# Kernel optimization log

Hardware: AMD Instinct MI355X
Metric: run time of the kernel (lower is better)

Reference implementation:

```python
import jax, jax.numpy as jnp
import numpy as np

N = 50000      # nodes
E = 800000     # directed edges (before self loops)
B = 64         # graphs in batch
F_IN = 128     # input_dim
POS = 16       # pos_dim
H = 4          # heads
C = 64         # hidden_dim (per head)
HC = H * C     # 256
OUT = 128      # output_dim
ENH = F_IN + POS
EPS = 1e-5
NEG_SLOPE = 0.2


def setup_inputs() -> dict:
    key = jax.random.key(0)
    ks = jax.random.split(key, 20)
    s = 0.05
    inp = {
        "x": jax.random.normal(ks[0], (N, F_IN), jnp.float32),
        "edge_index": jax.random.randint(ks[1], (2, E), 0, N, jnp.int32),
        "batch": (jnp.arange(N, dtype=jnp.int32) // ((N + B - 1) // B)).astype(jnp.int32),
        "W_pos": jax.random.normal(ks[2], (2, POS), jnp.float32) * s,
        "b_pos": jnp.zeros((POS,), jnp.float32),
        "W1": jax.random.normal(ks[3], (ENH, HC), jnp.float32) * s,
        "a_src1": jax.random.normal(ks[4], (H, C), jnp.float32) * s,
        "a_dst1": jax.random.normal(ks[5], (H, C), jnp.float32) * s,
        "b1": jnp.zeros((HC,), jnp.float32),
        "gamma1": jnp.ones((HC,), jnp.float32),
        "beta1": jnp.zeros((HC,), jnp.float32),
        "W2": jax.random.normal(ks[6], (HC, HC), jnp.float32) * s,
        "a_src2": jax.random.normal(ks[7], (H, C), jnp.float32) * s,
        "a_dst2": jax.random.normal(ks[8], (H, C), jnp.float32) * s,
        "b2": jnp.zeros((HC,), jnp.float32),
        "gamma2": jnp.ones((HC,), jnp.float32),
        "beta2": jnp.zeros((HC,), jnp.float32),
        "W_fc": jax.random.normal(ks[9], (HC, OUT), jnp.float32) * s,
        "b_fc": jnp.zeros((OUT,), jnp.float32),
    }
    return inp


def _positions(batch):
    # vectorized equivalent of _generate_positions (grid layout per graph)
    ones = jnp.ones((N,), jnp.float32)
    counts = jax.ops.segment_sum(ones, batch, num_segments=B)          # [B]
    starts = jnp.cumsum(counts) - counts                               # [B]
    i = jnp.arange(N, dtype=jnp.float32) - starts[batch]               # index within graph
    gs = jnp.ceil(jnp.sqrt(counts)).astype(jnp.int32)                  # grid size per graph
    g = gs[batch]
    ii = i.astype(jnp.int32)
    row = ii // g
    col = ii % g
    denom = jnp.maximum(g - 1, 1).astype(jnp.float32)
    return jnp.stack([row.astype(jnp.float32) / denom,
                      col.astype(jnp.float32) / denom], axis=1)        # [N, 2]


def _gat(x, W, a_src, a_dst, bias, src, dst):
    # PyG GATConv (concat heads, add_self_loops already in src/dst)
    h = (x @ W).reshape(N, H, C)                                       # [N,H,C]
    alpha_s = jnp.sum(h * a_src, axis=-1)                              # [N,H]
    alpha_d = jnp.sum(h * a_dst, axis=-1)                              # [N,H]
    e = jax.nn.leaky_relu(alpha_s[src] + alpha_d[dst], NEG_SLOPE)      # [Etot,H]
    e_max = jax.ops.segment_max(e, dst, num_segments=N)                # [N,H]
    e_max = jax.lax.stop_gradient(jnp.where(jnp.isfinite(e_max), e_max, 0.0))
    ex = jnp.exp(e - e_max[dst])
    denom = jax.ops.segment_sum(ex, dst, num_segments=N)               # [N,H]
    alpha = ex / denom[dst]                                            # softmax over incoming edges
    msg = h[src] * alpha[:, :, None]                                   # [Etot,H,C]
    out = jax.ops.segment_sum(msg, dst, num_segments=N)                # [N,H,C]
    return out.reshape(N, HC) + bias


def _bn(x, gamma, beta):
    m = jnp.mean(x, axis=0)
    v = jnp.var(x, axis=0)
    return gamma * (x - m) * jax.lax.rsqrt(v + EPS) + beta


def reference(x, edge_index, batch, W_pos, b_pos,
              W1, a_src1, a_dst1, b1, gamma1, beta1,
              W2, a_src2, a_dst2, b2, gamma2, beta2,
              W_fc, b_fc):
    pos = _positions(batch)
    pe = pos @ W_pos + b_pos                                           # [N,POS]
    h = jnp.concatenate([x, pe], axis=1)                               # [N,ENH]
    loops = jnp.arange(N, dtype=edge_index.dtype)
    src = jnp.concatenate([edge_index[0], loops])
    dst = jnp.concatenate([edge_index[1], loops])
    h = jax.nn.elu(_bn(_gat(h, W1, a_src1, a_dst1, b1, src, dst), gamma1, beta1))
    h = jax.nn.elu(_bn(_gat(h, W2, a_src2, a_dst2, b2, src, dst), gamma2, beta2))
    # global mean pool per graph
    counts = jax.ops.segment_sum(jnp.ones((N,), h.dtype), batch, num_segments=B)
    pooled = jax.ops.segment_sum(h, batch, num_segments=B) / counts[:, None]
    return pooled @ W_fc + b_fc                                        # [B,OUT]
```

## Files before the change

kernel.cpp:

```cpp
#include <hip/hip_runtime.h>
#include <math.h>

#define POSD 16
#define DEG_CAP 64
#define NSLICE 16
#define AGG_BLOCKS 2048

typedef __attribute__((ext_vector_type(8))) __bf16 bf16x8;
typedef __attribute__((ext_vector_type(4))) float f32x4;

__device__ __forceinline__ unsigned short f2bf(float f){
  unsigned int u = __float_as_uint(f);
  u += 0x7FFF + ((u >> 16) & 1);
  return (unsigned short)(u >> 16);
}
__device__ __forceinline__ float bf2f(unsigned short u){
  return __uint_as_float(((unsigned int)u) << 16);
}

__global__ __launch_bounds__(256) void k_init(
    const int* __restrict__ batch, int* __restrict__ starts,
    const int* __restrict__ src, const int* __restrict__ dst,
    int* __restrict__ cnt, int* __restrict__ csr_src,
    float* __restrict__ bnP, float* __restrict__ pooled,
    const float* __restrict__ x, unsigned short* __restrict__ xb,
    const float* __restrict__ W_pos, const float* __restrict__ b_pos,
    const float* __restrict__ W1, const float* __restrict__ W2,
    unsigned short* __restrict__ W1t, unsigned short* __restrict__ W2t,
    float* __restrict__ uvw,
    int N, int E, int nfb, int nxb){
  int bx = blockIdx.x;
  int t = threadIdx.x;
  if (bx < nfb){
    int i = bx * 256 + t;
    if (i < 2 * NSLICE * 512) bnP[i] = 0.f;
    if (i < 64 * 256) pooled[i] = 0.f;
    if (i < N){
      int bi = batch[i];
      int bp = (i == 0) ? -1 : batch[i - 1];
      for (int b = bp + 1; b <= bi; ++b) starts[b] = i;
      if (i == N - 1){
        for (int b = bi + 1; b <= 64; ++b) starts[b] = N;
      }
    }
    if (i < E){
      int d = dst[i];
      int slot = atomicAdd(&cnt[d], 1);
      csr_src[(size_t)d * DEG_CAP + slot] = src[i];
    }
  } else if (bx < nfb + nxb){
    size_t idx8 = (size_t)(bx - nfb) * 256 + t;
    if (idx8 * 8 < (size_t)N * 128){
      const float4* xs = (const float4*)(x + idx8 * 8);
      float4 v0 = xs[0], v1 = xs[1];
      ushort4 o0, o1;
      o0.x = f2bf(v0.x); o0.y = f2bf(v0.y); o0.z = f2bf(v0.z); o0.w = f2bf(v0.w);
      o1.x = f2bf(v1.x); o1.y = f2bf(v1.y); o1.z = f2bf(v1.z); o1.w = f2bf(v1.w);
      ushort4* od = (ushort4*)(xb + idx8 * 8);
      od[0] = o0; od[1] = o1;
    }
  } else if (bx < nfb + nxb + 128){
    int idx = (bx - nfb - nxb) * 256 + t;
    int n = idx >> 7, k = idx & 127;
    W1t[idx] = f2bf(W1[(size_t)k * 256 + n]);
  } else if (bx < nfb + nxb + 128 + 256){
    int j = (bx - nfb - nxb - 128) * 256 + t;
    int n = j >> 8, k = j & 255;
    W2t[j] = f2bf(W2[(size_t)k * 256 + n]);
  } else {
    float u = 0.f, v = 0.f, wv = 0.f;
    #pragma unroll
    for (int k = 0; k < POSD; ++k){
      float wc = W1[(size_t)(128 + k) * 256 + t];
      u  += W_pos[k] * wc;
      v  += W_pos[POSD + k] * wc;
      wv += b_pos[k] * wc;
    }
    uvw[t] = u; uvw[256 + t] = v; uvw[512 + t] = wv;
  }
}

#define LDST 40
template<int POSC>
__global__ __launch_bounds__(256) void k_mfma_gemm(
    const unsigned short* __restrict__ A, const unsigned short* __restrict__ Bt,
    unsigned short* __restrict__ C,
    const float* __restrict__ a_src, const float* __restrict__ a_dst,
    float* __restrict__ alpS, float* __restrict__ alpD, int M, int Kp,
    const float* __restrict__ uvw, const int* __restrict__ batch,
    const int* __restrict__ starts){
  __shared__ unsigned short As[128 * LDST];
  __shared__ unsigned short Bs[128 * LDST];
  int t = threadIdx.x;
  int lane = t & 63, wave = t >> 6;
  int wm = (wave >> 1) * 64, wn = (wave & 1) * 64;
  int quad = lane >> 4, l16 = lane & 15;
  int row0 = blockIdx.x * 128;
  int n0 = blockIdx.y * 128;

  f32x4 acc[4][4] = {};

  int eA0 = t, eA1 = t + 256;
  for (int kk = 0; kk < Kp; kk += 32){
    #pragma unroll
    for (int rep = 0; rep < 2; ++rep){
      int e = rep ? eA1 : eA0;
      int r = e >> 2, s = e & 3;
      int grow = row0 + r;
      uint4 va = make_uint4(0, 0, 0, 0);
      if (grow < M) va = *(const uint4*)(A + (size_t)grow * Kp + kk + s * 8);
      *(uint4*)&As[r * LDST + s * 8] = va;
      uint4 vb = *(const uint4*)(Bt + (size_t)(n0 + r) * Kp + kk + s * 8);
      *(uint4*)&Bs[r * LDST + s * 8] = vb;
    }
    __syncthreads();
    bf16x8 af[4], bfr[4];
    #pragma unroll
    for (int i = 0; i < 4; ++i)
      af[i] = *(const bf16x8*)&As[(wm + i * 16 + l16) * LDST + quad * 8];
    #pragma unroll
    for (int j = 0; j < 4; ++j)
      bfr[j] = *(const bf16x8*)&Bs[(wn + j * 16 + l16) * LDST + quad * 8];
    #pragma unroll
    for (int i = 0; i < 4; ++i)
      #pragma unroll
      for (int j = 0; j < 4; ++j)
        acc[i][j] = __builtin_amdgcn_mfma_f32_16x16x32_bf16(af[i], bfr[j], acc[i][j], 0, 0, 0);
    __syncthreads();
  }

  if (POSC){
    float uu[4], vv[4], ww[4];
    #pragma unroll
    for (int j = 0; j < 4; ++j){
      int col = n0 + wn + j * 16 + l16;
      uu[j] = uvw[col]; vv[j] = uvw[256 + col]; ww[j] = uvw[512 + col];
    }
    #pragma unroll
    for (int i = 0; i < 4; ++i){
      #pragma unroll
      for (int r = 0; r < 4; ++r){
        int row = row0 + wm + i * 16 + quad * 4 + r;
        if (row < M){
          int b = batch[row];
          int st = starts[b];
          int cc = starts[b + 1] - st;
          int g2 = (int)ceilf(sqrtf((float)cc));
          int dd = g2 - 1; if (dd < 1) dd = 1;
          float idn = 1.0f / (float)dd;
          int ii = row - st;
          int irow = ii / g2;
          int icol = ii - irow * g2;
          float rn = (float)irow * idn, cn = (float)icol * idn;
          #pragma unroll
          for (int j = 0; j < 4; ++j)
            acc[i][j][r] += rn * uu[j] + cn * vv[j] + ww[j];
        }
      }
    }
  }

  #pragma unroll
  for (int i = 0; i < 4; ++i){
    int rbase = row0 + wm + i * 16 + quad * 4;
    #pragma unroll
    for (int j = 0; j < 4; ++j){
      int col = n0 + wn + j * 16 + l16;
      #pragma unroll
      for (int r = 0; r < 4; ++r){
        int row = rbase + r;
        if (row < M) C[(size_t)row * 256 + col] = f2bf(acc[i][j][r]);
      }
    }
  }
  int hda = (n0 + wn) >> 6;
  float asw[4], adw[4];
  #pragma unroll
  for (int j = 0; j < 4; ++j){
    int c = n0 + wn + j * 16 + l16;
    asw[j] = a_src[c];
    adw[j] = a_dst[c];
  }
  #pragma unroll
  for (int i = 0; i < 4; ++i){
    #pragma unroll
    for (int r = 0; r < 4; ++r){
      int row = row0 + wm + i * 16 + quad * 4 + r;
      float ps = acc[i][0][r] * asw[0] + acc[i][1][r] * asw[1]
               + acc[i][2][r] * asw[2] + acc[i][3][r] * asw[3];
      float pd = acc[i][0][r] * adw[0] + acc[i][1][r] * adw[1]
               + acc[i][2][r] * adw[2] + acc[i][3][r] * adw[3];
      ps += __shfl_xor(ps, 1); ps += __shfl_xor(ps, 2);
      ps += __shfl_xor(ps, 4); ps += __shfl_xor(ps, 8);
      pd += __shfl_xor(pd, 1); pd += __shfl_xor(pd, 2);
      pd += __shfl_xor(pd, 4); pd += __shfl_xor(pd, 8);
      if (l16 == 0 && row < M){
        alpS[row * 4 + hda] = ps;
        alpD[row * 4 + hda] = pd;
      }
    }
  }
}

__global__ __launch_bounds__(256) void k_aggregate(const unsigned short* __restrict__ hlin,
                                                   const float* __restrict__ alpS,
                                                   const float* __restrict__ alpD,
                                                   const int* __restrict__ cnt,
                                                   const int* __restrict__ csr_src,
                                                   const float* __restrict__ bias,
                                                   unsigned short* __restrict__ outb,
                                                   float* __restrict__ bnP,
                                                   int N, int ngroups){
  __shared__ float rs[4][256];
  __shared__ float rq[4][256];
  int wv = threadIdx.x >> 6;
  int lane = threadIdx.x & 63;
  int hd = lane >> 4;
  int hd2 = lane & 3;
  int eloc = lane >> 2;
  const unsigned short* hbase = hlin + (size_t)lane * 4;
  float4 bv = *(const float4*)(bias + lane * 4);

  float s0 = 0.f, s1 = 0.f, s2 = 0.f, s3 = 0.f;
  float q0 = 0.f, q1 = 0.f, q2 = 0.f, q3 = 0.f;

  for (int grp = blockIdx.x; grp < ngroups; grp += gridDim.x){
    int n = grp * 4 + wv;
    if (n < N){
      int beg = n << 6;
      int deg = cnt[n];
      int total = deg + 1;
      float ad2 = alpD[n * 4 + hd2];
      float lsum = 0.f;
      float a0 = 0.f, a1 = 0.f, a2 = 0.f, a3 = 0.f;

      int full = total & ~15;
      for (int base = 0; base < full; base += 16){
        int e = base + eloc;
        int s = (e < deg) ? csr_src[beg + e] : n;
        float xv = alpS[s * 4 + hd2] + ad2;
        float sc = (xv >= 0.f) ? xv : 0.2f * xv;
        float p = __expf(sc);
        lsum += p;
        uint2 v[16];
        #pragma unroll
        for (int j2 = 0; j2 < 16; ++j2){
          int sj = __shfl(s, j2 << 2);
          v[j2] = *(const uint2*)(hbase + (size_t)sj * 256);
        }
        #pragma unroll
        for (int j2 = 0; j2 < 16; ++j2){
          float pj = __shfl(p, (j2 << 2) | hd);
          a0 += pj * __uint_as_float(v[j2].x << 16);
          a1 += pj * __uint_as_float(v[j2].x & 0xFFFF0000u);
          a2 += pj * __uint_as_float(v[j2].y << 16);
          a3 += pj * __uint_as_float(v[j2].y & 0xFFFF0000u);
        }
      }
      int rem = total - full;
      if (rem){
        int e = full + eloc;
        int s = n;
        float p = 0.f;
        if (eloc < rem){
          if (e < deg) s = csr_src[beg + e];
          float xv = alpS[s * 4 + hd2] + ad2;
          float sc = (xv >= 0.f) ? xv : 0.2f * xv;
          p = __expf(sc);
        }
        lsum += p;
        #pragma unroll
        for (int g = 0; g < 4; ++g){
          if (g * 4 < rem){
            uint2 v[4];
            #pragma unroll
            for (int q = 0; q < 4; ++q){
              int j2 = g * 4 + q;
              int sj = __shfl(s, j2 << 2);
              v[q] = *(const uint2*)(hbase + (size_t)sj * 256);
            }
            #pragma unroll
            for (int q = 0; q < 4; ++q){
              int j2 = g * 4 + q;
              float pj = __shfl(p, (j2 << 2) | hd);
              a0 += pj * __uint_as_float(v[q].x << 16);
              a1 += pj * __uint_as_float(v[q].x & 0xFFFF0000u);
              a2 += pj * __uint_as_float(v[q].y << 16);
              a3 += pj * __uint_as_float(v[q].y & 0xFFFF0000u);
            }
          }
        }
      }
      lsum += __shfl_xor(lsum, 4);
      lsum += __shfl_xor(lsum, 8);
      lsum += __shfl_xor(lsum, 16);
      lsum += __shfl_xor(lsum, 32);
      float lh = __shfl(lsum, hd);
      float inv = 1.0f / lh;
      ushort4 o;
      o.x = f2bf(a0 * inv + bv.x);
      o.y = f2bf(a1 * inv + bv.y);
      o.z = f2bf(a2 * inv + bv.z);
      o.w = f2bf(a3 * inv + bv.w);
      *(ushort4*)(outb + (size_t)n * 256 + lane * 4) = o;
      float f0 = bf2f(o.x), f1 = bf2f(o.y), f2 = bf2f(o.z), f3 = bf2f(o.w);
      s0 += f0; s1 += f1; s2 += f2; s3 += f3;
      q0 += f0 * f0; q1 += f1 * f1; q2 += f2 * f2; q3 += f3 * f3;
    }
  }

  int c0 = lane * 4;
  rs[wv][c0 + 0] = s0; rs[wv][c0 + 1] = s1;
  rs[wv][c0 + 2] = s2; rs[wv][c0 + 3] = s3;
  rq[wv][c0 + 0] = q0; rq[wv][c0 + 1] = q1;
  rq[wv][c0 + 2] = q2; rq[wv][c0 + 3] = q3;
  __syncthreads();
  int t = threadIdx.x;
  float s = rs[0][t] + rs[1][t] + rs[2][t] + rs[3][t];
  float q = rq[0][t] + rq[1][t] + rq[2][t] + rq[3][t];
  float* bp = bnP + (size_t)(blockIdx.x & (NSLICE - 1)) * 512;
  atomicAdd(&bp[t], s);
  atomicAdd(&bp[256 + t], q);
}

__global__ __launch_bounds__(256) void k_bn_elu_bf16(
    const unsigned short* __restrict__ in, const float* __restrict__ bnP,
    const float* __restrict__ gamma, const float* __restrict__ beta,
    unsigned short* __restrict__ outb, int N, float invN){
  __shared__ float scs[256], shs[256];
  int t = threadIdx.x;
  float s = 0.f, q = 0.f;
  #pragma unroll
  for (int j = 0; j < NSLICE; ++j){
    s += bnP[j * 512 + t];
    q += bnP[j * 512 + 256 + t];
  }
  float mean = s * invN;
  float var = q * invN - mean * mean;
  float inv = rsqrtf(var + 1e-5f);
  float g = gamma[t];
  scs[t] = g * inv;
  shs[t] = beta[t] - mean * g * inv;
  __syncthreads();
  int idx8 = blockIdx.x * blockDim.x + t;
  int total8 = N * 32;
  for (; idx8 < total8; idx8 += gridDim.x * blockDim.x){
    int c0 = (idx8 * 8) & 255;
    uint4 raw = *(const uint4*)(in + (size_t)idx8 * 8);
    unsigned int rw[4] = {raw.x, raw.y, raw.z, raw.w};
    uint4 outw;
    unsigned int* ow = (unsigned int*)&outw;
    #pragma unroll
    for (int h = 0; h < 4; ++h){
      unsigned int res = 0;
      #pragma unroll
      for (int k = 0; k < 2; ++k){
        int c = c0 + h * 2 + k;
        unsigned short bits = (unsigned short)((rw[h] >> (16 * k)) & 0xFFFF);
        float y = scs[c] * bf2f(bits) + shs[c];
        y = (y > 0.f) ? y : (__expf(y) - 1.f);
        res |= ((unsigned int)f2bf(y)) << (16 * k);
      }
      ow[h] = res;
    }
    *(uint4*)(outb + (size_t)idx8 * 8) = outw;
  }
}

__global__ __launch_bounds__(256) void k_bn_elu_pool(
    const unsigned short* __restrict__ in, const float* __restrict__ bnP,
    const float* __restrict__ gamma, const float* __restrict__ beta,
    const int* __restrict__ batch,
    float* __restrict__ pooled, int N, float invN){
  int t = threadIdx.x;
  float s = 0.f, q = 0.f;
  #pragma unroll
  for (int j = 0; j < NSLICE; ++j){
    s += bnP[j * 512 + t];
    q += bnP[j * 512 + 256 + t];
  }
  float mean = s * invN;
  float var = q * invN - mean * mean;
  float inv = rsqrtf(var + 1e-5f);
  float g = gamma[t];
  float scl = g * inv;
  float shf = beta[t] - mean * scl;
  int nb = gridDim.x;
  int rows = (N + nb - 1) / nb;
  int r0 = blockIdx.x * rows, r1 = min(r0 + rows, N);
  float acc = 0.f; int cur = -1;
  for (int r = r0; r < r1; ++r){
    float y = scl * bf2f(in[(size_t)r * 256 + t]) + shf;
    y = (y > 0.f) ? y : (__expf(y) - 1.f);
    int b = batch[r];
    if (b != cur){
      if (cur >= 0) atomicAdd(&pooled[cur * 256 + t], acc);
      acc = 0.f; cur = b;
    }
    acc += y;
  }
  if (cur >= 0) atomicAdd(&pooled[cur * 256 + t], acc);
}

__global__ __launch_bounds__(128) void k_final(const float* __restrict__ pooled,
                                               const int* __restrict__ starts,
                                               const float* __restrict__ W_fc,
                                               const float* __restrict__ b_fc,
                                               float* __restrict__ out){
  __shared__ float pm[256];
  int b = blockIdx.x;
  int t = threadIdx.x;
  int c = starts[b + 1] - starts[b];
  float ic = (c > 0) ? 1.0f / (float)c : 0.f;
  pm[t] = pooled[b * 256 + t] * ic;
  pm[t + 128] = pooled[b * 256 + t + 128] * ic;
  __syncthreads();
  float acc = b_fc[t];
  #pragma unroll 4
  for (int cc = 0; cc < 256; ++cc) acc += pm[cc] * W_fc[cc * 128 + t];
  out[b * 128 + t] = acc;
}

extern "C" void kernel_launch(void* const* d_in, const int* in_sizes, int n_in,
                              void* d_out, int out_size, void* d_ws, size_t ws_size,
                              hipStream_t stream){
  const float* x      = (const float*)d_in[0];
  const int*   eidx   = (const int*)  d_in[1];
  const int*   batch  = (const int*)  d_in[2];
  const float* W_pos  = (const float*)d_in[3];
  const float* b_pos  = (const float*)d_in[4];
  const float* W1     = (const float*)d_in[5];
  const float* a_src1 = (const float*)d_in[6];
  const float* a_dst1 = (const float*)d_in[7];
  const float* b1     = (const float*)d_in[8];
  const float* gamma1 = (const float*)d_in[9];
  const float* beta1  = (const float*)d_in[10];
  const float* W2     = (const float*)d_in[11];
  const float* a_src2 = (const float*)d_in[12];
  const float* a_dst2 = (const float*)d_in[13];
  const float* b2     = (const float*)d_in[14];
  const float* gamma2 = (const float*)d_in[15];
  const float* beta2  = (const float*)d_in[16];
  const float* W_fc   = (const float*)d_in[17];
  const float* b_fc   = (const float*)d_in[18];
  float* out = (float*)d_out;

  const int N = in_sizes[0] / 128;
  const int E = in_sizes[1] / 2;
  const int* esrc = eidx;
  const int* edst = eidx + E;

  char* w = (char*)d_ws;
  size_t off = 0;
  auto alloc = [&](size_t bytes) -> void* {
    void* p = w + off;
    off = (off + bytes + 255) & ~(size_t)255;
    return p;
  };
  unsigned short* xb   = (unsigned short*)alloc((size_t)N * 128 * 2);
  unsigned short* X1b  = (unsigned short*)alloc((size_t)N * 256 * 2);
  unsigned short* A1b  = (unsigned short*)alloc((size_t)N * 256 * 2);
  unsigned short* X2b  = (unsigned short*)alloc((size_t)N * 256 * 2);
  float* alpS    = (float*)alloc((size_t)N * 4 * 4);
  float* alpD    = (float*)alloc((size_t)N * 4 * 4);
  int*   starts  = (int*)  alloc(65 * 4);
  int*   cnt     = (int*)  alloc((size_t)N * 4);
  int*   csr_src = (int*)  alloc((size_t)N * DEG_CAP * 4);
  float* bnP     = (float*)alloc((size_t)2 * NSLICE * 512 * 4);
  float* pooled  = (float*)alloc(64 * 256 * 4);
  unsigned short* W1t = (unsigned short*)alloc(256 * 128 * 2);
  unsigned short* W2t = (unsigned short*)alloc(256 * 256 * 2);
  float* uvw = (float*)alloc(3 * 256 * 4);
  float* bnP1 = bnP, *bnP2 = bnP + NSLICE * 512;

  hipMemsetAsync(cnt, 0, (size_t)N * 4, stream);

  const int nfb = (E + 255) / 256;
  const int nxb = ((N * 128 / 8) + 255) / 256;
  const int ngroups = (N + 3) / 4;

  k_init<<<nfb + nxb + 128 + 256 + 1, 256, 0, stream>>>(
      batch, starts, esrc, edst, cnt, csr_src, bnP, pooled,
      x, xb, W_pos, b_pos, W1, W2, W1t, W2t, uvw, N, E, nfb, nxb);

  dim3 ggrid((N + 127) / 128, 2);
  const float invN = 1.0f / (float)N;

  k_mfma_gemm<1><<<ggrid, 256, 0, stream>>>(xb, W1t, X1b, a_src1, a_dst1,
                                            alpS, alpD, N, 128, uvw, batch, starts);
  k_aggregate<<<AGG_BLOCKS, 256, 0, stream>>>(X1b, alpS, alpD, cnt, csr_src, b1,
                                              A1b, bnP1, N, ngroups);
  k_bn_elu_bf16<<<512, 256, 0, stream>>>(A1b, bnP1, gamma1, beta1, X2b, N, invN);

  k_mfma_gemm<0><<<ggrid, 256, 0, stream>>>(X2b, W2t, X1b, a_src2, a_dst2,
                                            alpS, alpD, N, 256, nullptr, nullptr, nullptr);
  k_aggregate<<<AGG_BLOCKS, 256, 0, stream>>>(X1b, alpS, alpD, cnt, csr_src, b2,
                                              A1b, bnP2, N, ngroups);
  k_bn_elu_pool<<<512, 256, 0, stream>>>(A1b, bnP2, gamma2, beta2, batch, pooled, N, invN);

  k_final<<<64, 128, 0, stream>>>(pooled, starts, W_fc, b_fc, out);
}
```

Before: 416.9 us.

## Fuse x bf16 conversion into first GEMM and merge pooling with final FC

Removes the separate fp32-to-bf16 pass over x by converting inside the first GEMM's shared-memory tile load, eliminating the xb buffer round trip. Replaces the BN/ELU/pool kernel with atomics plus the separate FC kernel with a single per-graph kernel that reduces rows in shared memory and applies W_fc. The tail now runs only 64 blocks over the full activation matrix, which may underuse the GPU compared to the previous 512-block pooling.

```diff
diff --git a/kernel.cpp b/kernel.cpp
--- a/kernel.cpp
+++ b/kernel.cpp
@@ -22,19 +22,17 @@
     const int* __restrict__ batch, int* __restrict__ starts,
     const int* __restrict__ src, const int* __restrict__ dst,
     int* __restrict__ cnt, int* __restrict__ csr_src,
-    float* __restrict__ bnP, float* __restrict__ pooled,
-    const float* __restrict__ x, unsigned short* __restrict__ xb,
+    float* __restrict__ bnP,
     const float* __restrict__ W_pos, const float* __restrict__ b_pos,
     const float* __restrict__ W1, const float* __restrict__ W2,
     unsigned short* __restrict__ W1t, unsigned short* __restrict__ W2t,
     float* __restrict__ uvw,
-    int N, int E, int nfb, int nxb){
+    int N, int E, int nfb){
   int bx = blockIdx.x;
   int t = threadIdx.x;
   if (bx < nfb){
     int i = bx * 256 + t;
     if (i < 2 * NSLICE * 512) bnP[i] = 0.f;
-    if (i < 64 * 256) pooled[i] = 0.f;
     if (i < N){
       int bi = batch[i];
       int bp = (i == 0) ? -1 : batch[i - 1];
@@ -48,23 +46,12 @@
       int slot = atomicAdd(&cnt[d], 1);
       csr_src[(size_t)d * DEG_CAP + slot] = src[i];
     }
-  } else if (bx < nfb + nxb){
-    size_t idx8 = (size_t)(bx - nfb) * 256 + t;
-    if (idx8 * 8 < (size_t)N * 128){
-      const float4* xs = (const float4*)(x + idx8 * 8);
-      float4 v0 = xs[0], v1 = xs[1];
-      ushort4 o0, o1;
-      o0.x = f2bf(v0.x); o0.y = f2bf(v0.y); o0.z = f2bf(v0.z); o0.w = f2bf(v0.w);
-      o1.x = f2bf(v1.x); o1.y = f2bf(v1.y); o1.z = f2bf(v1.z); o1.w = f2bf(v1.w);
-      ushort4* od = (ushort4*)(xb + idx8 * 8);
-      od[0] = o0; od[1] = o1;
-    }
-  } else if (bx < nfb + nxb + 128){
-    int idx = (bx - nfb - nxb) * 256 + t;
+  } else if (bx < nfb + 128){
+    int idx = (bx - nfb) * 256 + t;
     int n = idx >> 7, k = idx & 127;
     W1t[idx] = f2bf(W1[(size_t)k * 256 + n]);
-  } else if (bx < nfb + nxb + 128 + 256){
-    int j = (bx - nfb - nxb - 128) * 256 + t;
+  } else if (bx < nfb + 128 + 256){
+    int j = (bx - nfb - 128) * 256 + t;
     int n = j >> 8, k = j & 255;
     W2t[j] = f2bf(W2[(size_t)k * 256 + n]);
   } else {
@@ -83,7 +70,8 @@
 #define LDST 40
 template<int POSC>
 __global__ __launch_bounds__(256) void k_mfma_gemm(
-    const unsigned short* __restrict__ A, const unsigned short* __restrict__ Bt,
+    const unsigned short* __restrict__ A, const float* __restrict__ Af,
+    const unsigned short* __restrict__ Bt,
     unsigned short* __restrict__ C,
     const float* __restrict__ a_src, const float* __restrict__ a_dst,
     float* __restrict__ alpS, float* __restrict__ alpD, int M, int Kp,
@@ -107,9 +95,22 @@
       int e = rep ? eA1 : eA0;
       int r = e >> 2, s = e & 3;
       int grow = row0 + r;
-      uint4 va = make_uint4(0, 0, 0, 0);
-      if (grow < M) va = *(const uint4*)(A + (size_t)grow * Kp + kk + s * 8);
-      *(uint4*)&As[r * LDST + s * 8] = va;
+      if (POSC){
+        float4 f0 = make_float4(0.f, 0.f, 0.f, 0.f), f1 = f0;
+        if (grow < M){
+          const float4* xs = (const float4*)(Af + (size_t)grow * Kp + kk + s * 8);
+          f0 = xs[0]; f1 = xs[1];
+        }
+        ushort4 o0, o1;
+        o0.x = f2bf(f0.x); o0.y = f2bf(f0.y); o0.z = f2bf(f0.z); o0.w = f2bf(f0.w);
+        o1.x = f2bf(f1.x); o1.y = f2bf(f1.y); o1.z = f2bf(f1.z); o1.w = f2bf(f1.w);
+        *(ushort4*)&As[r * LDST + s * 8] = o0;
+        *(ushort4*)&As[r * LDST + s * 8 + 4] = o1;
+      } else {
+        uint4 va = make_uint4(0, 0, 0, 0);
+        if (grow < M) va = *(const uint4*)(A + (size_t)grow * Kp + kk + s * 8);
+        *(uint4*)&As[r * LDST + s * 8] = va;
+      }
       uint4 vb = *(const uint4*)(Bt + (size_t)(n0 + r) * Kp + kk + s * 8);
       *(uint4*)&Bs[r * LDST + s * 8] = vb;
     }
@@ -367,58 +368,55 @@
   }
 }
 
-__global__ __launch_bounds__(256) void k_bn_elu_pool(
+__global__ __launch_bounds__(1024) void k_tail(
     const unsigned short* __restrict__ in, const float* __restrict__ bnP,
     const float* __restrict__ gamma, const float* __restrict__ beta,
-    const int* __restrict__ batch,
-    float* __restrict__ pooled, int N, float invN){
+    const int* __restrict__ starts, const float* __restrict__ W_fc,
+    const float* __restrict__ b_fc, float* __restrict__ out, float invN){
+  __shared__ float pm[4][256];
+  __shared__ float scs[256], shs[256];
   int t = threadIdx.x;
-  float s = 0.f, q = 0.f;
-  #pragma unroll
-  for (int j = 0; j < NSLICE; ++j){
-    s += bnP[j * 512 + t];
-    q += bnP[j * 512 + 256 + t];
-  }
-  float mean = s * invN;
-  float var = q * invN - mean * mean;
-  float inv = rsqrtf(var + 1e-5f);
-  float g = gamma[t];
-  float scl = g * inv;
-  float shf = beta[t] - mean * scl;
-  int nb = gridDim.x;
-  int rows = (N + nb - 1) / nb;
-  int r0 = blockIdx.x * rows, r1 = min(r0 + rows, N);
-  float acc = 0.f; int cur = -1;
-  for (int r = r0; r < r1; ++r){
-    float y = scl * bf2f(in[(size_t)r * 256 + t]) + shf;
+  int c = t & 255;
+  int seg = t >> 8;
+  if (t < 256){
+    float s = 0.f, q = 0.f;
+    #pragma unroll
+    for (int j = 0; j < NSLICE; ++j){
+      s += bnP[j * 512 + t];
+      q += bnP[j * 512 + 256 + t];
+    }
+    float mean = s * invN;
+    float var = q * invN - mean * mean;
+    float inv = rsqrtf(var + 1e-5f);
+    float g = gamma[t];
+    scs[t] = g * inv;
+    shs[t] = beta[t] - mean * g * inv;
+  }
+  __syncthreads();
+  int b = blockIdx.x;
+  int r0 = starts[b], r1 = starts[b + 1];
+  float scl = scs[c], shf = shs[c];
+  float acc = 0.f;
+  #pragma unroll 4
+  for (int r = r0 + seg; r < r1; r += 4){
+    float y = scl * bf2f(in[(size_t)r * 256 + c]) + shf;
     y = (y > 0.f) ? y : (__expf(y) - 1.f);
-    int b = batch[r];
-    if (b != cur){
-      if (cur >= 0) atomicAdd(&pooled[cur * 256 + t], acc);
-      acc = 0.f; cur = b;
-    }
     acc += y;
   }
-  if (cur >= 0) atomicAdd(&pooled[cur * 256 + t], acc);
-}
-
-__global__ __launch_bounds__(128) void k_final(const float* __restrict__ pooled,
-                                               const int* __restrict__ starts,
-                                               const float* __restrict__ W_fc,
-                                               const float* __restrict__ b_fc,
-                                               float* __restrict__ out){
-  __shared__ float pm[256];
-  int b = blockIdx.x;
-  int t = threadIdx.x;
-  int c = starts[b + 1] - starts[b];
-  float ic = (c > 0) ? 1.0f / (float)c : 0.f;
-  pm[t] = pooled[b * 256 + t] * ic;
-  pm[t + 128] = pooled[b * 256 + t + 128] * ic;
+  pm[seg][c] = acc;
   __syncthreads();
-  float acc = b_fc[t];
-  #pragma unroll 4
-  for (int cc = 0; cc < 256; ++cc) acc += pm[cc] * W_fc[cc * 128 + t];
-  out[b * 128 + t] = acc;
+  if (t < 256){
+    int cnt = r1 - r0;
+    float ic = (cnt > 0) ? 1.0f / (float)cnt : 0.f;
+    pm[0][t] = (pm[0][t] + pm[1][t] + pm[2][t] + pm[3][t]) * ic;
+  }
+  __syncthreads();
+  if (t < 128){
+    float a = b_fc[t];
+    #pragma unroll 4
+    for (int cc = 0; cc < 256; ++cc) a += pm[0][cc] * W_fc[cc * 128 + t];
+    out[b * 128 + t] = a;
+  }
 }
 
 extern "C" void kernel_launch(void* const* d_in, const int* in_sizes, int n_in,
@@ -457,7 +455,6 @@
     off = (off + bytes + 255) & ~(size_t)255;
     return p;
   };
-  unsigned short* xb   = (unsigned short*)alloc((size_t)N * 128 * 2);
   unsigned short* X1b  = (unsigned short*)alloc((size_t)N * 256 * 2);
   unsigned short* A1b  = (unsigned short*)alloc((size_t)N * 256 * 2);
   unsigned short* X2b  = (unsigned short*)alloc((size_t)N * 256 * 2);
@@ -467,7 +464,6 @@
   int*   cnt     = (int*)  alloc((size_t)N * 4);
   int*   csr_src = (int*)  alloc((size_t)N * DEG_CAP * 4);
   float* bnP     = (float*)alloc((size_t)2 * NSLICE * 512 * 4);
-  float* pooled  = (float*)alloc(64 * 256 * 4);
   unsigned short* W1t = (unsigned short*)alloc(256 * 128 * 2);
   unsigned short* W2t = (unsigned short*)alloc(256 * 256 * 2);
   float* uvw = (float*)alloc(3 * 256 * 4);
@@ -476,27 +472,26 @@
   hipMemsetAsync(cnt, 0, (size_t)N * 4, stream);
 
   const int nfb = (E + 255) / 256;
-  const int nxb = ((N * 128 / 8) + 255) / 256;
   const int ngroups = (N + 3) / 4;
 
-  k_init<<<nfb + nxb + 128 + 256 + 1, 256, 0, stream>>>(
-      batch, starts, esrc, edst, cnt, csr_src, bnP, pooled,
-      x, xb, W_pos, b_pos, W1, W2, W1t, W2t, uvw, N, E, nfb, nxb);
+  k_init<<<nfb + 128 + 256 + 1, 256, 0, stream>>>(
+      batch, starts, esrc, edst, cnt, csr_src, bnP,
+      W_pos, b_pos, W1, W2, W1t, W2t, uvw, N, E, nfb);
 
   dim3 ggrid((N + 127) / 128, 2);
   const float invN = 1.0f / (float)N;
 
-  k_mfma_gemm<1><<<ggrid, 256, 0, stream>>>(xb, W1t, X1b, a_src1, a_dst1,
+  k_mfma_gemm<1><<<ggrid, 256, 0, stream>>>(nullptr, x, W1t, X1b, a_src1, a_dst1,
                                             alpS, alpD, N, 128, uvw, batch, starts);
   k_aggregate<<<AGG_BLOCKS, 256, 0, stream>>>(X1b, alpS, alpD, cnt, csr_src, b1,
                                               A1b, bnP1, N, ngroups);
   k_bn_elu_bf16<<<512, 256, 0, stream>>>(A1b, bnP1, gamma1, beta1, X2b, N, invN);
 
-  k_mfma_gemm<0><<<ggrid, 256, 0, stream>>>(X2b, W2t, X1b, a_src2, a_dst2,
+  k_mfma_gemm<0><<<ggrid, 256, 0, stream>>>(X2b, nullptr, W2t, X1b, a_src2, a_dst2,
                                             alpS, alpD, N, 256, nullptr, nullptr, nullptr);
   k_aggregate<<<AGG_BLOCKS, 256, 0, stream>>>(X1b, alpS, alpD, cnt, csr_src, b2,
                                               A1b, bnP2, N, ngroups);
-  k_bn_elu_pool<<<512, 256, 0, stream>>>(A1b, bnP2, gamma2, beta2, batch, pooled, N, invN);
-
-  k_final<<<64, 128, 0, stream>>>(pooled, starts, W_fc, b_fc, out);
-}
+
+  k_tail<<<64, 1024, 0, stream>>>(A1b, bnP2, gamma2, beta2, starts, W_fc, b_fc,
+                                  out, invN);
+}
```

Result: faster. 398.8 us (-4.3%).
